# Optimization experiments

Hardware: AMD Instinct MI355X
Metric: run time of the kernel (lower is better)

Reference implementation:

```python
import jax, jax.numpy as jnp
import numpy as np

B, T, L, S, D = 32, 32, 196, 512, 512


def setup_inputs() -> dict:
    key = jax.random.key(0)
    ks = jax.random.split(key, 8)
    sc = 0.05
    return {
        "x": jax.random.normal(ks[0], (B, T, D), jnp.float32),
        "x_static": jax.random.normal(ks[1], (B, L, S), jnp.float32),
        "h0": jnp.zeros((B, D), jnp.float32),
        "W1": jax.random.normal(ks[2], (S, D), jnp.float32) * sc,
        "W2": jax.random.normal(ks[3], (D, D), jnp.float32) * sc,
        "W3": jax.random.normal(ks[4], (D + S, D), jnp.float32) * sc,
        "b2": jax.random.normal(ks[5], (D,), jnp.float32) * sc,
        "b3": jax.random.normal(ks[6], (D,), jnp.float32) * sc,
        "V": jax.random.normal(ks[7], (D, 1), jnp.float32) * sc,
    }


def reference(x, x_static, h0, W1, W2, W3, b2, b3, V):
    # Precompute static projection once (Bahdanau precompute): [B, L, D]
    total = jnp.einsum("bls,sd->bld", x_static, W1) + b2

    def step(h, x_t):
        # h: [B, D] previous output; x_t: [B, D] current word feature
        hw = h @ W2                                   # [B, D]
        additive = total + hw[:, None, :]             # [B, L, D]
        scores = jnp.einsum("bld,do->blo", additive, V)  # [B, L, 1]
        attn = jax.nn.softmax(scores, axis=1)         # [B, L, 1]
        ctx = jnp.sum(attn * x_static, axis=1)        # [B, S]
        new_h = jnp.concatenate([x_t, ctx], axis=1) @ W3 + b3  # [B, D]
        return new_h, new_h

    _, outputs = jax.lax.scan(step, h0, jnp.swapaxes(x, 0, 1))  # [T, B, D]
    return jnp.swapaxes(outputs, 0, 1)  # [B, T, D]
```

## Files before the change

### kernel.cpp

```cpp
#include <hip/hip_runtime.h>
#include <math.h>

#define B 32
#define T 32
#define L 196
#define S 512
#define D 512

__global__ void k_w1v(const float* __restrict__ W1, const float* __restrict__ V,
                      float* __restrict__ w1v) {
    const int wave = threadIdx.x >> 6, lane = threadIdx.x & 63;
    const int row  = blockIdx.x * 4 + wave;
    const float4* r  = (const float4*)(W1 + (size_t)row * D);
    const float4* v4 = (const float4*)V;
    float p0 = 0.f, p1 = 0.f;
    {
        float4 a = r[lane], bb = v4[lane];
        p0 = a.x * bb.x + a.y * bb.y + a.z * bb.z + a.w * bb.w;
        float4 c = r[64 + lane], dd = v4[64 + lane];
        p1 = c.x * dd.x + c.y * dd.y + c.z * dd.z + c.w * dd.w;
    }
    float p = p0 + p1;
    for (int off = 32; off; off >>= 1) p += __shfl_down(p, off);
    if (lane == 0) w1v[row] = p;
}

__global__ void k_scores(const float* __restrict__ xs, const float* __restrict__ w1v,
                         float* __restrict__ sc) {
    const int wave = threadIdx.x >> 6, lane = threadIdx.x & 63;
    const int row  = blockIdx.x * 4 + wave;
    if (row >= B * L) return;
    const float4* r  = (const float4*)(xs + (size_t)row * S);
    const float4* v4 = (const float4*)w1v;
    float4 a = r[lane], bb = v4[lane];
    float4 c = r[64 + lane], dd = v4[64 + lane];
    float p = (a.x * bb.x + a.y * bb.y + a.z * bb.z + a.w * bb.w) +
              (c.x * dd.x + c.y * dd.y + c.z * dd.z + c.w * dd.w);
    for (int off = 32; off; off >>= 1) p += __shfl_down(p, off);
    if (lane == 0) sc[row] = p;
}

__global__ void k_ctx(const float* __restrict__ xs, const float* __restrict__ sc,
                      float* __restrict__ ctx) {
    __shared__ float attn[256];
    __shared__ float red[8];
    __shared__ float part[4][64];
    const int b = blockIdx.y, s0 = blockIdx.x * 64, tid = threadIdx.x;
    const int lane = tid & 63, wave = tid >> 6;

    float v = (tid < L) ? sc[b * L + tid] : -1e30f;
    float m = v;
    for (int off = 32; off; off >>= 1) m = fmaxf(m, __shfl_down(m, off));
    if (lane == 0) red[wave] = m;
    __syncthreads();
    m = fmaxf(fmaxf(red[0], red[1]), fmaxf(red[2], red[3]));
    float e = (tid < L) ? expf(v - m) : 0.f;
    attn[tid] = e;
    float ssum = e;
    for (int off = 32; off; off >>= 1) ssum += __shfl_down(ssum, off);
    if (lane == 0) red[4 + wave] = ssum;
    __syncthreads();
    const float inv = 1.f / (red[4] + red[5] + red[6] + red[7]);

    const float* xb = xs + (size_t)b * L * S + s0 + lane;
    float a[8];
#pragma unroll
    for (int u = 0; u < 8; ++u) a[u] = 0.f;
    int l = wave;
    for (int g = 0; g < 6; ++g) {
#pragma unroll
        for (int u = 0; u < 8; ++u)
            a[u] = fmaf(attn[l + u * 4], xb[(size_t)(l + u * 4) * S], a[u]);
        l += 32;
    }
    a[0] = fmaf(attn[l], xb[(size_t)l * S], a[0]);
    float acc = ((a[0] + a[1]) + (a[2] + a[3])) + ((a[4] + a[5]) + (a[6] + a[7]));
    part[wave][lane] = acc;
    __syncthreads();
    if (wave == 0)
        ctx[b * S + s0 + lane] =
            (part[0][lane] + part[1][lane] + part[2][lane] + part[3][lane]) * inv;
}

__global__ void k_cproj(const float* __restrict__ ctx, const float* __restrict__ W3,
                        const float* __restrict__ b3, float* __restrict__ cp) {
    __shared__ float c[S];
    __shared__ float part[4][64];
    const int b = blockIdx.y, d0 = blockIdx.x * 64, tid = threadIdx.x;
    const int lane = tid & 63, sub = tid >> 6;
    for (int i = tid; i < S; i += 256) c[i] = ctx[b * S + i];
    __syncthreads();

    const float* w = W3 + (size_t)D * D + d0 + lane;
    float a[8];
#pragma unroll
    for (int u = 0; u < 8; ++u) a[u] = 0.f;
    const int sbase = sub * 128;
    for (int s = sbase; s < sbase + 128; s += 8) {
#pragma unroll
        for (int u = 0; u < 8; ++u)
            a[u] = fmaf(c[s + u], w[(size_t)(s + u) * D], a[u]);
    }
    float acc = ((a[0] + a[1]) + (a[2] + a[3])) + ((a[4] + a[5]) + (a[6] + a[7]));
    part[sub][lane] = acc;
    __syncthreads();
    if (sub == 0)
        cp[b * D + d0 + lane] = part[0][lane] + part[1][lane] + part[2][lane] +
                                part[3][lane] + b3[d0 + lane];
}

__global__ __launch_bounds__(256) void k_out(const float* __restrict__ x,
                                             const float* __restrict__ W3,
                                             const float* __restrict__ cp,
                                             float* __restrict__ out) {
    __shared__ float xlt[D * 4];
    const int b = blockIdx.z, t0 = blockIdx.y * 4, d0 = blockIdx.x * 256;
    const int tid = threadIdx.x;
    const float* xb = x + ((size_t)b * T + t0) * D;
    for (int idx = tid; idx < 4 * D; idx += 256) {
        const int i = idx >> 9;
        const int k = idx & (D - 1);
        xlt[k * 4 + i] = xb[(size_t)i * D + k];
    }
    __syncthreads();

    const int d = d0 + tid;
    const float* wp = W3 + d;
    float a0 = 0.f, a1 = 0.f, a2 = 0.f, a3 = 0.f;
#pragma unroll 16
    for (int k = 0; k < D; ++k) {
        const float w  = wp[(size_t)k * D];
        const float4 xv = *(const float4*)&xlt[k * 4];
        a0 = fmaf(xv.x, w, a0);
        a1 = fmaf(xv.y, w, a1);
        a2 = fmaf(xv.z, w, a2);
        a3 = fmaf(xv.w, w, a3);
    }
    const float c = cp[b * D + d];
    float* ob = out + ((size_t)b * T + t0) * D + d;
    ob[0 * D] = a0 + c;
    ob[1 * D] = a1 + c;
    ob[2 * D] = a2 + c;
    ob[3 * D] = a3 + c;
}

extern "C" void kernel_launch(void* const* d_in, const int* in_sizes, int n_in,
                              void* d_out, int out_size, void* d_ws, size_t ws_size,
                              hipStream_t stream) {
    const float* x  = (const float*)d_in[0];
    const float* xs = (const float*)d_in[1];
    const float* W1 = (const float*)d_in[3];
    const float* W3 = (const float*)d_in[5];
    const float* b3 = (const float*)d_in[7];
    const float* V  = (const float*)d_in[8];
    float* out = (float*)d_out;

    float* ws  = (float*)d_ws;
    float* w1v = ws;
    float* sc  = ws + 512;
    float* cp  = ws;
    float* ctx = ws + 16384;

    k_w1v   <<<dim3(S / 4),       dim3(256), 0, stream>>>(W1, V, w1v);
    k_scores<<<dim3(B * L / 4),   dim3(256), 0, stream>>>(xs, w1v, sc);
    k_ctx   <<<dim3(S / 64, B),   dim3(256), 0, stream>>>(xs, sc, ctx);
    k_cproj <<<dim3(D / 64, B),   dim3(256), 0, stream>>>(ctx, W3, b3, cp);
    k_out   <<<dim3(2, T / 4, B), dim3(256), 0, stream>>>(x, W3, cp, out);
}
```

Before: 109.4 us.

## Fuse context and context-projection kernels, retile output GEMM with split-K

Merges the context kernel and the W3 context projection into one 512-thread kernel. Each block now writes a partial projection over its 64-wide slice of S, and those partials are summed together with the bias inside the output kernel. The output kernel now handles 8 timesteps per block, uses float4 weight loads, and splits K across 4 waves with a shared-memory reduction. The goals are to remove one launch, improve weight reuse, and raise arithmetic intensity. In exchange it adds partial-sum traffic, uses much more shared memory (48KB), which may lower occupancy, and halves the number of output blocks.

```diff
diff --git a/kernel.cpp b/kernel.cpp
--- a/kernel.cpp
+++ b/kernel.cpp
@@ -13,14 +13,10 @@
     const int row  = blockIdx.x * 4 + wave;
     const float4* r  = (const float4*)(W1 + (size_t)row * D);
     const float4* v4 = (const float4*)V;
-    float p0 = 0.f, p1 = 0.f;
-    {
-        float4 a = r[lane], bb = v4[lane];
-        p0 = a.x * bb.x + a.y * bb.y + a.z * bb.z + a.w * bb.w;
-        float4 c = r[64 + lane], dd = v4[64 + lane];
-        p1 = c.x * dd.x + c.y * dd.y + c.z * dd.z + c.w * dd.w;
-    }
-    float p = p0 + p1;
+    float4 a = r[lane], bb = v4[lane];
+    float4 c = r[64 + lane], dd = v4[64 + lane];
+    float p = (a.x * bb.x + a.y * bb.y + a.z * bb.z + a.w * bb.w) +
+              (c.x * dd.x + c.y * dd.y + c.z * dd.z + c.w * dd.w);
     for (int off = 32; off; off >>= 1) p += __shfl_down(p, off);
     if (lane == 0) w1v[row] = p;
 }
@@ -40,11 +36,14 @@
     if (lane == 0) sc[row] = p;
 }
 
-__global__ void k_ctx(const float* __restrict__ xs, const float* __restrict__ sc,
-                      float* __restrict__ ctx) {
-    __shared__ float attn[256];
-    __shared__ float red[8];
-    __shared__ float part[4][64];
+__global__ __launch_bounds__(512) void k_ctx_cp(const float* __restrict__ xs,
+                                                const float* __restrict__ sc,
+                                                const float* __restrict__ W3,
+                                                float* __restrict__ cpp) {
+    __shared__ float attn[512];
+    __shared__ float red[16];
+    __shared__ float part[8][64];
+    __shared__ float cs[64];
     const int b = blockIdx.y, s0 = blockIdx.x * 64, tid = threadIdx.x;
     const int lane = tid & 63, wave = tid >> 6;
 
@@ -53,95 +52,105 @@
     for (int off = 32; off; off >>= 1) m = fmaxf(m, __shfl_down(m, off));
     if (lane == 0) red[wave] = m;
     __syncthreads();
-    m = fmaxf(fmaxf(red[0], red[1]), fmaxf(red[2], red[3]));
+    m = fmaxf(fmaxf(fmaxf(red[0], red[1]), fmaxf(red[2], red[3])),
+              fmaxf(fmaxf(red[4], red[5]), fmaxf(red[6], red[7])));
     float e = (tid < L) ? expf(v - m) : 0.f;
     attn[tid] = e;
     float ssum = e;
     for (int off = 32; off; off >>= 1) ssum += __shfl_down(ssum, off);
-    if (lane == 0) red[4 + wave] = ssum;
+    if (lane == 0) red[8 + wave] = ssum;
     __syncthreads();
-    const float inv = 1.f / (red[4] + red[5] + red[6] + red[7]);
+    const float inv = 1.f / (red[8] + red[9] + red[10] + red[11] +
+                             red[12] + red[13] + red[14] + red[15]);
 
     const float* xb = xs + (size_t)b * L * S + s0 + lane;
     float a[8];
 #pragma unroll
     for (int u = 0; u < 8; ++u) a[u] = 0.f;
     int l = wave;
-    for (int g = 0; g < 6; ++g) {
+    for (int g = 0; g < 3; ++g) {
 #pragma unroll
         for (int u = 0; u < 8; ++u)
-            a[u] = fmaf(attn[l + u * 4], xb[(size_t)(l + u * 4) * S], a[u]);
-        l += 32;
+            a[u] = fmaf(attn[l + u * 8], xb[(size_t)(l + u * 8) * S], a[u]);
+        l += 64;
     }
-    a[0] = fmaf(attn[l], xb[(size_t)l * S], a[0]);
+    if (wave < 4)
+        a[0] = fmaf(attn[l], xb[(size_t)l * S], a[0]);
     float acc = ((a[0] + a[1]) + (a[2] + a[3])) + ((a[4] + a[5]) + (a[6] + a[7]));
     part[wave][lane] = acc;
     __syncthreads();
-    if (wave == 0)
-        ctx[b * S + s0 + lane] =
-            (part[0][lane] + part[1][lane] + part[2][lane] + part[3][lane]) * inv;
-}
-
-__global__ void k_cproj(const float* __restrict__ ctx, const float* __restrict__ W3,
-                        const float* __restrict__ b3, float* __restrict__ cp) {
-    __shared__ float c[S];
-    __shared__ float part[4][64];
-    const int b = blockIdx.y, d0 = blockIdx.x * 64, tid = threadIdx.x;
-    const int lane = tid & 63, sub = tid >> 6;
-    for (int i = tid; i < S; i += 256) c[i] = ctx[b * S + i];
+    if (wave == 0) {
+        float t = ((part[0][lane] + part[1][lane]) + (part[2][lane] + part[3][lane])) +
+                  ((part[4][lane] + part[5][lane]) + (part[6][lane] + part[7][lane]));
+        cs[lane] = t * inv;
+    }
     __syncthreads();
 
-    const float* w = W3 + (size_t)D * D + d0 + lane;
-    float a[8];
+    const float* wr = W3 + ((size_t)(D + s0)) * D + tid;
+    float a2[4] = {0.f, 0.f, 0.f, 0.f};
 #pragma unroll
-    for (int u = 0; u < 8; ++u) a[u] = 0.f;
-    const int sbase = sub * 128;
-    for (int s = sbase; s < sbase + 128; s += 8) {
+    for (int s = 0; s < 64; s += 4) {
 #pragma unroll
-        for (int u = 0; u < 8; ++u)
-            a[u] = fmaf(c[s + u], w[(size_t)(s + u) * D], a[u]);
+        for (int u = 0; u < 4; ++u)
+            a2[u] = fmaf(cs[s + u], wr[(size_t)(s + u) * D], a2[u]);
     }
-    float acc = ((a[0] + a[1]) + (a[2] + a[3])) + ((a[4] + a[5]) + (a[6] + a[7]));
-    part[sub][lane] = acc;
-    __syncthreads();
-    if (sub == 0)
-        cp[b * D + d0 + lane] = part[0][lane] + part[1][lane] + part[2][lane] +
-                                part[3][lane] + b3[d0 + lane];
+    cpp[((size_t)b * 8 + blockIdx.x) * D + tid] = (a2[0] + a2[1]) + (a2[2] + a2[3]);
 }
 
 __global__ __launch_bounds__(256) void k_out(const float* __restrict__ x,
                                              const float* __restrict__ W3,
-                                             const float* __restrict__ cp,
+                                             const float* __restrict__ cpp,
+                                             const float* __restrict__ b3,
                                              float* __restrict__ out) {
-    __shared__ float xlt[D * 4];
-    const int b = blockIdx.z, t0 = blockIdx.y * 4, d0 = blockIdx.x * 256;
-    const int tid = threadIdx.x;
+    __shared__ float xlt[D * 8];
+    __shared__ float red[4 * 8 * 256];
+    const int b = blockIdx.z, t0 = blockIdx.y * 8, d0 = blockIdx.x * 256;
+    const int tid = threadIdx.x, lane = tid & 63, wave = tid >> 6;
+
     const float* xb = x + ((size_t)b * T + t0) * D;
-    for (int idx = tid; idx < 4 * D; idx += 256) {
-        const int i = idx >> 9;
+    for (int idx = tid; idx < 8 * D; idx += 256) {
+        const int t = idx >> 9;
         const int k = idx & (D - 1);
-        xlt[k * 4 + i] = xb[(size_t)i * D + k];
+        xlt[k * 8 + t] = xb[(size_t)t * D + k];
     }
     __syncthreads();
 
-    const int d = d0 + tid;
-    const float* wp = W3 + d;
-    float a0 = 0.f, a1 = 0.f, a2 = 0.f, a3 = 0.f;
-#pragma unroll 16
-    for (int k = 0; k < D; ++k) {
-        const float w  = wp[(size_t)k * D];
-        const float4 xv = *(const float4*)&xlt[k * 4];
-        a0 = fmaf(xv.x, w, a0);
-        a1 = fmaf(xv.y, w, a1);
-        a2 = fmaf(xv.z, w, a2);
-        a3 = fmaf(xv.w, w, a3);
+    const int kbeg = wave * 128;
+    const float* wp = W3 + (size_t)kbeg * D + d0 + (lane << 2);
+    float4 acc[8];
+#pragma unroll
+    for (int t = 0; t < 8; ++t) acc[t] = make_float4(0.f, 0.f, 0.f, 0.f);
+
+#pragma unroll 8
+    for (int kk = 0; kk < 128; ++kk) {
+        const float4 w4 = *(const float4*)(wp + (size_t)kk * D);
+        const float4 xa = *(const float4*)&xlt[(kbeg + kk) * 8];
+        const float4 xc = *(const float4*)&xlt[(kbeg + kk) * 8 + 4];
+        const float xt[8] = {xa.x, xa.y, xa.z, xa.w, xc.x, xc.y, xc.z, xc.w};
+#pragma unroll
+        for (int t = 0; t < 8; ++t) {
+            acc[t].x = fmaf(xt[t], w4.x, acc[t].x);
+            acc[t].y = fmaf(xt[t], w4.y, acc[t].y);
+            acc[t].z = fmaf(xt[t], w4.z, acc[t].z);
+            acc[t].w = fmaf(xt[t], w4.w, acc[t].w);
+        }
     }
-    const float c = cp[b * D + d];
-    float* ob = out + ((size_t)b * T + t0) * D + d;
-    ob[0 * D] = a0 + c;
-    ob[1 * D] = a1 + c;
-    ob[2 * D] = a2 + c;
-    ob[3 * D] = a3 + c;
+
+    float* rw = red + ((wave * 8) << 8) + (lane << 2);
+#pragma unroll
+    for (int t = 0; t < 8; ++t) *(float4*)(rw + (t << 8)) = acc[t];
+    __syncthreads();
+
+    float cpsum = b3[d0 + tid];
+#pragma unroll
+    for (int j = 0; j < 8; ++j) cpsum += cpp[((size_t)b * 8 + j) * D + d0 + tid];
+    float* ob = out + ((size_t)b * T + t0) * D + d0 + tid;
+#pragma unroll
+    for (int t = 0; t < 8; ++t) {
+        const float v = (red[(0 * 8 + t) * 256 + tid] + red[(1 * 8 + t) * 256 + tid]) +
+                        (red[(2 * 8 + t) * 256 + tid] + red[(3 * 8 + t) * 256 + tid]);
+        ob[(size_t)t * D] = v + cpsum;
+    }
 }
 
 extern "C" void kernel_launch(void* const* d_in, const int* in_sizes, int n_in,
@@ -158,12 +167,10 @@
     float* ws  = (float*)d_ws;
     float* w1v = ws;
     float* sc  = ws + 512;
-    float* cp  = ws;
-    float* ctx = ws + 16384;
+    float* cpp = ws + 8192;
 
-    k_w1v   <<<dim3(S / 4),       dim3(256), 0, stream>>>(W1, V, w1v);
-    k_scores<<<dim3(B * L / 4),   dim3(256), 0, stream>>>(xs, w1v, sc);
-    k_ctx   <<<dim3(S / 64, B),   dim3(256), 0, stream>>>(xs, sc, ctx);
-    k_cproj <<<dim3(D / 64, B),   dim3(256), 0, stream>>>(ctx, W3, b3, cp);
-    k_out   <<<dim3(2, T / 4, B), dim3(256), 0, stream>>>(x, W3, cp, out);
+    k_w1v   <<<dim3(S / 4),         dim3(256), 0, stream>>>(W1, V, w1v);
+    k_scores<<<dim3(B * L / 4),     dim3(256), 0, stream>>>(xs, w1v, sc);
+    k_ctx_cp<<<dim3(S / 64, B),     dim3(512), 0, stream>>>(xs, sc, W3, cpp);
+    k_out   <<<dim3(2, T / 8, B),   dim3(256), 0, stream>>>(x, W3, cpp, b3, out);
 }
```

Result: faster. 101.3 us (-7.4%).
